# Kernel tuning notes

Measured on AMD Instinct MI355X. Metric: run time of the kernel, lower is better.

Reference implementation:

```python
import jax, jax.numpy as jnp
import numpy as np

LOG_CLAMP = -100.0  # torch BCE clamps log terms at -100


def _weights_from_target(target):
    # target: [B, 1, W, W]; weight[b,i,j] = W / (sqrt((i-x)^2 + (j-y)^2) + 1)
    # where (x, y) is the mean location of the per-sample max of target.
    B = target.shape[0]
    W = target.shape[-1]
    t = target.reshape(B, W, W)
    m = jnp.max(t, axis=(1, 2), keepdims=True)
    mask = (t == m).astype(t.dtype)                      # all argmax locations
    cnt = jnp.sum(mask, axis=(1, 2))                     # [B]
    idx = jnp.arange(W, dtype=t.dtype)
    x = jnp.sum(mask * idx[None, :, None], axis=(1, 2)) / cnt  # mean row index
    y = jnp.sum(mask * idx[None, None, :], axis=(1, 2)) / cnt  # mean col index
    a = idx[None, :, None] - x[:, None, None]            # [B, W, 1]
    b = idx[None, None, :] - y[:, None, None]            # [B, 1, W]
    dist = (jnp.sqrt(a * a + b * b) + 1.0) / W           # [B, W, W]
    return (1.0 / dist).reshape(target.shape)


def reference(input, target):
    weights = _weights_from_target(target)
    log_p = jnp.maximum(jnp.log(input), LOG_CLAMP)
    log_1mp = jnp.maximum(jnp.log1p(-input), LOG_CLAMP)
    bce = -(target * log_p + (1.0 - target) * log_1mp)
    return jnp.mean(weights * bce)


def setup_inputs() -> dict:
    key = jax.random.key(0)
    k1, k2 = jax.random.split(key)
    shape = (256, 1, 224, 224)
    # BCE requires probabilities in (0,1); keep strictly inside via small margin.
    input = jax.random.uniform(k1, shape, dtype=jnp.float32, minval=1e-4, maxval=1.0 - 1e-4)
    target = jax.random.uniform(k2, shape, dtype=jnp.float32)
    return {"input": input, "target": target}
```

## Files before the change

kernel.cpp:

```cpp
#include <hip/hip_runtime.h>
#include <hip/hip_fp16.h>
#include <math.h>


#define WIMG 224
#define WW (WIMG * WIMG)
#define NQ (WW / 4)
#define NB 256
#define NT 1024
#define NIT (NQ / NT)
#define REM (NQ - NIT * NT)
#define LN2 0.69314718055994530942f
#define CLAMP2 (-144.269504088896340736f)

__device__ __forceinline__ void stat_upd(float val, float fi, float fj,
                                         float& m, float& cnt, float& si, float& sj)
{
    bool gt = val > m;
    bool eq = val == m;
    cnt = gt ? 1.0f : (cnt + (eq ? 1.0f : 0.0f));
    si  = gt ? fi   : (si  + (eq ? fi   : 0.0f));
    sj  = gt ? fj   : (sj  + (eq ? fj   : 0.0f));
    m   = fmaxf(m, val);
}

__global__ __launch_bounds__(NT, 4) void floss_kernel(
    const float* __restrict__ input,
    const float* __restrict__ target,
    float* __restrict__ out,
    float inv_total)
{
    const int b   = blockIdx.x;
    const int tid = threadIdx.x;
    const float4* __restrict__ t4 = (const float4*)(target + (size_t)b * WW);
    const float4* __restrict__ p4 = (const float4*)(input  + (size_t)b * WW);

    float m = -1.0f, cnt = 0.0f, si = 0.0f, sj = 0.0f;
    __half2 tc[2 * (NIT + 1)];
    #pragma unroll
    for (int it = 0; it < NIT; ++it) {
        int q = it * NT + tid;
        float4 v = t4[q];
        int i  = q / 56;
        int j0 = (q - i * 56) * 4;
        float fi = (float)i;
        stat_upd(v.x, fi, (float)(j0 + 0), m, cnt, si, sj);
        stat_upd(v.y, fi, (float)(j0 + 1), m, cnt, si, sj);
        stat_upd(v.z, fi, (float)(j0 + 2), m, cnt, si, sj);
        stat_upd(v.w, fi, (float)(j0 + 3), m, cnt, si, sj);
        tc[2 * it]     = __floats2half2_rn(v.x, v.y);
        tc[2 * it + 1] = __floats2half2_rn(v.z, v.w);
    }
    const bool has_tail = tid < REM;
    const int qt = NIT * NT + tid;
    if (has_tail) {
        float4 v = t4[qt];
        int i  = qt / 56;
        int j0 = (qt - i * 56) * 4;
        float fi = (float)i;
        stat_upd(v.x, fi, (float)(j0 + 0), m, cnt, si, sj);
        stat_upd(v.y, fi, (float)(j0 + 1), m, cnt, si, sj);
        stat_upd(v.z, fi, (float)(j0 + 2), m, cnt, si, sj);
        stat_upd(v.w, fi, (float)(j0 + 3), m, cnt, si, sj);
        tc[2 * NIT]     = __floats2half2_rn(v.x, v.y);
        tc[2 * NIT + 1] = __floats2half2_rn(v.z, v.w);
    }

    #pragma unroll
    for (int off = 32; off > 0; off >>= 1) {
        float m2  = __shfl_down(m,   off);
        float c2  = __shfl_down(cnt, off);
        float si2 = __shfl_down(si,  off);
        float sj2 = __shfl_down(sj,  off);
        bool gt = m2 > m, eq = m2 == m;
        cnt = gt ? c2  : (cnt + (eq ? c2  : 0.0f));
        si  = gt ? si2 : (si  + (eq ? si2 : 0.0f));
        sj  = gt ? sj2 : (sj  + (eq ? sj2 : 0.0f));
        m   = fmaxf(m, m2);
    }
    __shared__ float sm[16], sc[16], ssi[16], ssj[16];
    __shared__ float sxy[2];
    const int lane = tid & 63, wid = tid >> 6;
    if (lane == 0) { sm[wid] = m; sc[wid] = cnt; ssi[wid] = si; ssj[wid] = sj; }
    __syncthreads();
    if (tid == 0) {
        float M = sm[0], C = sc[0], SI = ssi[0], SJ = ssj[0];
        #pragma unroll
        for (int w = 1; w < 16; ++w) {
            float mw = sm[w];
            bool gt = mw > M, eq = mw == M;
            C  = gt ? sc[w]  : (C  + (eq ? sc[w]  : 0.0f));
            SI = gt ? ssi[w] : (SI + (eq ? ssi[w] : 0.0f));
            SJ = gt ? ssj[w] : (SJ + (eq ? ssj[w] : 0.0f));
            M  = fmaxf(M, mw);
        }
        sxy[0] = SI / C;
        sxy[1] = SJ / C;
    }
    __syncthreads();
    const float x = sxy[0], y = sxy[1];
    const float Kc = -(float)WIMG * LN2;

    float acc = 0.0f;
    #pragma unroll
    for (int it = 0; it <= NIT; ++it) {
        int q = (it < NIT) ? (it * NT + tid) : qt;
        if (it == NIT && !has_tail) break;
        float4 pv = p4[q];
        float2 t01 = __half22float2(tc[2 * it]);
        float2 t23 = __half22float2(tc[2 * it + 1]);
        int i  = q / 56;
        int j0 = (q - i * 56) * 4;
        float di  = (float)i - x;
        float di2 = di * di;
        float tt[4] = {t01.x, t01.y, t23.x, t23.y};
        float pp[4] = {pv.x, pv.y, pv.z, pv.w};
        #pragma unroll
        for (int k = 0; k < 4; ++k) {
            float dj = (float)(j0 + k) - y;
            float s  = __builtin_amdgcn_sqrtf(di2 + dj * dj);
            float wf = Kc * __builtin_amdgcn_rcpf(s + 1.0f);
            float p = pp[k], t = tt[k];
            float lp2  = fmaxf(__builtin_amdgcn_logf(p),        CLAMP2);
            float l1p2 = fmaxf(__builtin_amdgcn_logf(1.0f - p), CLAMP2);
            acc += wf * (l1p2 + t * (lp2 - l1p2));
        }
    }

    #pragma unroll
    for (int off = 32; off > 0; off >>= 1) acc += __shfl_down(acc, off);
    __shared__ float sred[16];
    if (lane == 0) sred[wid] = acc;
    __syncthreads();
    if (tid == 0) {
        float ssum = 0.0f;
        #pragma unroll
        for (int w = 0; w < 16; ++w) ssum += sred[w];
        atomicAdd(out, ssum * inv_total);
    }
}

extern "C" void kernel_launch(void* const* d_in, const int* in_sizes, int n_in,
                              void* d_out, int out_size, void* d_ws, size_t ws_size,
                              hipStream_t stream) {
    const float* input  = (const float*)d_in[0];
    const float* target = (const float*)d_in[1];
    float* out = (float*)d_out;
    hipMemsetAsync(out, 0, sizeof(float), stream);
    const float inv_total = 1.0f / (256.0f * 224.0f * 224.0f);
    floss_kernel<<<NB, NT, 0, stream>>>(input, target, out, inv_total);
}
```

Baseline: 137.5 us.

## Compute BCE in the first pass and stash half-precision results in LDS

```diff
diff --git a/kernel.cpp b/kernel.cpp
--- a/kernel.cpp
+++ b/kernel.cpp
@@ -10,6 +10,7 @@
 #define NT 1024
 #define NIT (NQ / NT)
 #define REM (NQ - NIT * NT)
+#define LDS_BYTES (2 * NQ * 4)
 #define LN2 0.69314718055994530942f
 #define CLAMP2 (-144.269504088896340736f)
 
@@ -24,46 +25,59 @@
     m   = fmaxf(m, val);
 }
 
+__device__ __forceinline__ float bce2_elem(float p, float t)
+{
+    float lp2  = fmaxf(__builtin_amdgcn_logf(p),        CLAMP2);
+    float l1p2 = fmaxf(__builtin_amdgcn_logf(1.0f - p), CLAMP2);
+    return l1p2 + t * (lp2 - l1p2);
+}
+
 __global__ __launch_bounds__(NT, 4) void floss_kernel(
     const float* __restrict__ input,
     const float* __restrict__ target,
     float* __restrict__ out,
     float inv_total)
 {
+    extern __shared__ __half2 bce_lds[];
     const int b   = blockIdx.x;
     const int tid = threadIdx.x;
     const float4* __restrict__ t4 = (const float4*)(target + (size_t)b * WW);
     const float4* __restrict__ p4 = (const float4*)(input  + (size_t)b * WW);
 
     float m = -1.0f, cnt = 0.0f, si = 0.0f, sj = 0.0f;
-    __half2 tc[2 * (NIT + 1)];
-    #pragma unroll
+    #pragma unroll 4
     for (int it = 0; it < NIT; ++it) {
         int q = it * NT + tid;
-        float4 v = t4[q];
+        float4 tv = t4[q];
+        float4 pv = p4[q];
         int i  = q / 56;
         int j0 = (q - i * 56) * 4;
         float fi = (float)i;
-        stat_upd(v.x, fi, (float)(j0 + 0), m, cnt, si, sj);
-        stat_upd(v.y, fi, (float)(j0 + 1), m, cnt, si, sj);
-        stat_upd(v.z, fi, (float)(j0 + 2), m, cnt, si, sj);
-        stat_upd(v.w, fi, (float)(j0 + 3), m, cnt, si, sj);
-        tc[2 * it]     = __floats2half2_rn(v.x, v.y);
-        tc[2 * it + 1] = __floats2half2_rn(v.z, v.w);
+        stat_upd(tv.x, fi, (float)(j0 + 0), m, cnt, si, sj);
+        stat_upd(tv.y, fi, (float)(j0 + 1), m, cnt, si, sj);
+        stat_upd(tv.z, fi, (float)(j0 + 2), m, cnt, si, sj);
+        stat_upd(tv.w, fi, (float)(j0 + 3), m, cnt, si, sj);
+        float b0 = bce2_elem(pv.x, tv.x);
+        float b1 = bce2_elem(pv.y, tv.y);
+        float b2 = bce2_elem(pv.z, tv.z);
+        float b3 = bce2_elem(pv.w, tv.w);
+        bce_lds[q]      = __floats2half2_rn(b0, b1);
+        bce_lds[NQ + q] = __floats2half2_rn(b2, b3);
     }
     const bool has_tail = tid < REM;
     const int qt = NIT * NT + tid;
     if (has_tail) {
-        float4 v = t4[qt];
+        float4 tv = t4[qt];
+        float4 pv = p4[qt];
         int i  = qt / 56;
         int j0 = (qt - i * 56) * 4;
         float fi = (float)i;
-        stat_upd(v.x, fi, (float)(j0 + 0), m, cnt, si, sj);
-        stat_upd(v.y, fi, (float)(j0 + 1), m, cnt, si, sj);
-        stat_upd(v.z, fi, (float)(j0 + 2), m, cnt, si, sj);
-        stat_upd(v.w, fi, (float)(j0 + 3), m, cnt, si, sj);
-        tc[2 * NIT]     = __floats2half2_rn(v.x, v.y);
-        tc[2 * NIT + 1] = __floats2half2_rn(v.z, v.w);
+        stat_upd(tv.x, fi, (float)(j0 + 0), m, cnt, si, sj);
+        stat_upd(tv.y, fi, (float)(j0 + 1), m, cnt, si, sj);
+        stat_upd(tv.z, fi, (float)(j0 + 2), m, cnt, si, sj);
+        stat_upd(tv.w, fi, (float)(j0 + 3), m, cnt, si, sj);
+        bce_lds[qt]      = __floats2half2_rn(bce2_elem(pv.x, tv.x), bce2_elem(pv.y, tv.y));
+        bce_lds[NQ + qt] = __floats2half2_rn(bce2_elem(pv.z, tv.z), bce2_elem(pv.w, tv.w));
     }
 
     #pragma unroll
@@ -104,26 +118,21 @@
     float acc = 0.0f;
     #pragma unroll
     for (int it = 0; it <= NIT; ++it) {
+        if (it == NIT && !has_tail) break;
         int q = (it < NIT) ? (it * NT + tid) : qt;
-        if (it == NIT && !has_tail) break;
-        float4 pv = p4[q];
-        float2 t01 = __half22float2(tc[2 * it]);
-        float2 t23 = __half22float2(tc[2 * it + 1]);
+        float2 b01 = __half22float2(bce_lds[q]);
+        float2 b23 = __half22float2(bce_lds[NQ + q]);
         int i  = q / 56;
         int j0 = (q - i * 56) * 4;
         float di  = (float)i - x;
         float di2 = di * di;
-        float tt[4] = {t01.x, t01.y, t23.x, t23.y};
-        float pp[4] = {pv.x, pv.y, pv.z, pv.w};
+        float bb[4] = {b01.x, b01.y, b23.x, b23.y};
         #pragma unroll
         for (int k = 0; k < 4; ++k) {
             float dj = (float)(j0 + k) - y;
             float s  = __builtin_amdgcn_sqrtf(di2 + dj * dj);
             float wf = Kc * __builtin_amdgcn_rcpf(s + 1.0f);
-            float p = pp[k], t = tt[k];
-            float lp2  = fmaxf(__builtin_amdgcn_logf(p),        CLAMP2);
-            float l1p2 = fmaxf(__builtin_amdgcn_logf(1.0f - p), CLAMP2);
-            acc += wf * (l1p2 + t * (lp2 - l1p2));
+            acc += wf * bb[k];
         }
     }
 
@@ -146,7 +155,9 @@
     const float* input  = (const float*)d_in[0];
     const float* target = (const float*)d_in[1];
     float* out = (float*)d_out;
+    hipFuncSetAttribute((const void*)floss_kernel,
+                        hipFuncAttributeMaxDynamicSharedMemorySize, LDS_BYTES);
     hipMemsetAsync(out, 0, sizeof(float), stream);
     const float inv_total = 1.0f / (256.0f * 224.0f * 224.0f);
-    floss_kernel<<<NB, NT, 0, stream>>>(input, target, out, inv_total);
+    floss_kernel<<<NB, NT, LDS_BYTES, stream>>>(input, target, out, inv_total);
 }
```

Measured after the change: 124.9 us. -9.2%, faster.
